# Optimization experiments

Measured on AMD Instinct MI355X. Metric: run time of the kernel, lower is better.

The kernel has to match this reference:

```python
import jax, jax.numpy as jnp
import numpy as np

T, B, DIM, N = 2048, 16, 1024, 64


def setup_inputs() -> dict:
    key = jax.random.key(0)
    ks = jax.random.split(key, 6)
    # xavier-uniform-ish scale for [N, DIM] linear weights
    lim = float(np.sqrt(6.0 / (DIM + N)))
    mk = lambda k: jax.random.uniform(k, (N, DIM), jnp.float32, -lim, lim)
    return {
        "x": jax.random.normal(ks[0], (T, B, DIM), jnp.float32),
        "S": jnp.zeros((B, N, N), jnp.float32),
        "W_k": mk(ks[1]),
        "W_v": mk(ks[2]),
        "W_q": mk(ks[3]),
        "W_alpha": mk(ks[4]),
        "d_alpha": jnp.full((N,), 0.1, jnp.float32),
        "b_alpha": jnp.full((N,), 2.0, jnp.float32),
    }


def reference(x, S, W_k, W_v, W_q, W_alpha, d_alpha, b_alpha):
    # Projections for the whole sequence at once: [T, B, N]
    k_all = jnp.einsum('tbd,nd->tbn', x, W_k)
    v_all = jnp.einsum('tbd,nd->tbn', x, W_v)
    q_all = jnp.einsum('tbd,nd->tbn', x, W_q)
    a_all = jnp.einsum('tbd,nd->tbn', x, W_alpha)

    def step(S, inp):
        k, v, q, ax = inp  # each [B, N]
        retrieved = jnp.einsum('bij,bj->bi', S, k)                 # [B, N]
        alpha = jax.nn.sigmoid(ax + d_alpha * retrieved + b_alpha)  # [B, N]
        outer_vk = v[:, :, None] * k[:, None, :]                    # [B, N, N]
        S = alpha[:, :, None] * S + (1.0 - alpha[:, :, None]) * outer_vk
        out = jnp.einsum('bij,bj->bi', S, q)                        # [B, N]
        out = out * jax.nn.silu(out)
        return S, out

    S_final, output = jax.lax.scan(step, S, (k_all, v_all, q_all, a_all))
    return output, S_final
```

## Files before the change

kernel.cpp:

```cpp
#include <hip/hip_runtime.h>
#include <hip/hip_bf16.h>

#define T_STEPS 2048
#define BATCH 16
#define DIM 1024
#define NDIM 64
#define M_TOTAL (T_STEPS * BATCH)
#define STRIDE (BATCH * NDIM)
#define CH 32

typedef __attribute__((ext_vector_type(8))) short bf16x8;
typedef __attribute__((ext_vector_type(4))) float f32x4;
typedef __attribute__((ext_vector_type(2))) float f32x2;

#define NEG_LOG2E -1.44269504088896f

__device__ inline unsigned pk_bf(float lo, float hi) {
    __hip_bfloat162 h = __float22bfloat162_rn(float2{lo, hi});
    return *(unsigned*)&h;
}

template <int CTRL>
__device__ inline float dpp_add(float x) {
    int v = __builtin_amdgcn_update_dpp(0, __float_as_int(x), CTRL, 0xF, 0xF, true);
    return x + __int_as_float(v);
}
__device__ inline float red16(float x) {
    x = dpp_add<0xB1>(x);
    x = dpp_add<0x4E>(x);
    x = dpp_add<0x141>(x);
    x = dpp_add<0x140>(x);
    return x;
}
__device__ inline void red16x2(float& a, float& b) {
    a = dpp_add<0xB1>(a);  b = dpp_add<0xB1>(b);
    a = dpp_add<0x4E>(a);  b = dpp_add<0x4E>(b);
    a = dpp_add<0x141>(a); b = dpp_add<0x141>(b);
    a = dpp_add<0x140>(a); b = dpp_add<0x140>(b);
}

#define AS1 __attribute__((address_space(1)))
#define AS3 __attribute__((address_space(3)))
__device__ inline void gl_lds16(const float* g, float* l) {
    __builtin_amdgcn_global_load_lds((const AS1 unsigned*)g, (AS3 unsigned*)l, 16, 0, 0);
}
__device__ inline void gl_lds16s(const unsigned short* g, unsigned short* l) {
    __builtin_amdgcn_global_load_lds((const AS1 unsigned*)g, (AS3 unsigned*)l, 16, 0, 0);
}
__device__ inline void gl_lds4(const float* g, float* l) {
    __builtin_amdgcn_global_load_lds((const AS1 unsigned*)g, (AS3 unsigned*)l, 4, 0, 0);
}
#define WAIT_VM0 do { __builtin_amdgcn_s_waitcnt(0x0F70); asm volatile("" ::: "memory"); } while (0)

__global__ __launch_bounds__(256) void pack_w(
    const float* __restrict__ Wk, const float* __restrict__ Wq,
    const float* __restrict__ Wv, const float* __restrict__ Wa,
    unsigned short* __restrict__ Wb) {
    int n = blockIdx.x;
    int sel = n >> 6;
    const float* W = (sel == 0) ? Wk : (sel == 1) ? Wq : (sel == 2) ? Wv : Wa;
    int k4 = threadIdx.x * 4;
    float4 f = *(const float4*)(W + (size_t)(n & 63) * DIM + k4);
    uint2 u;
    u.x = pk_bf(f.x, f.y);
    u.y = pk_bf(f.z, f.w);
    *(uint2*)(Wb + (size_t)n * DIM + k4) = u;
}

__global__ __launch_bounds__(256, 2) void proj_kernel(
    const float* __restrict__ x, const unsigned short* __restrict__ Wb,
    const float* __restrict__ ba, float* __restrict__ Kp, float* __restrict__ Qp,
    float* __restrict__ VAi) {
    __shared__ float sA[128 * 64];
    __shared__ unsigned short sB[128 * 64];

    const int m0 = blockIdx.x * 128;
    const int ntile = blockIdx.y;
    const int tid = threadIdx.x;
    const int wv = tid >> 6, lane = tid & 63, lrow = lane & 15, quad = lane >> 4;
    const int wm = wv & 1, wn = wv >> 1;

    f32x4 acc[4][4];
#pragma unroll
    for (int a = 0; a < 4; a++)
#pragma unroll
        for (int b = 0; b < 4; b++) acc[a][b] = (f32x4)(0.f);

    const float* xg = x + (size_t)(m0 + (tid >> 4)) * DIM + (tid & 15) * 4;
    const unsigned short* wg = Wb + (size_t)(ntile * 128 + (tid >> 3)) * DIM + (tid & 7) * 8;

    for (int it = 0; it < 16; ++it) {
        const int k0 = it * 64;
        __syncthreads();
#pragma unroll
        for (int j = 0; j < 8; ++j)
            gl_lds16(xg + (size_t)(16 * j) * DIM + k0, &sA[(tid + 256 * j) * 4]);
#pragma unroll
        for (int j = 0; j < 4; ++j)
            gl_lds16s(wg + (size_t)(32 * j) * DIM + k0, &sB[(tid + 256 * j) * 8]);
        WAIT_VM0;
        __syncthreads();

#pragma unroll
        for (int ks = 0; ks < 2; ++ks) {
            bf16x8 af[4];
#pragma unroll
            for (int mt = 0; mt < 4; ++mt) {
                const float* pa = &sA[(wm * 64 + mt * 16 + lrow) * 64 + ks * 32 + quad * 8];
                float4 lo = ((const float4*)pa)[0], hi = ((const float4*)pa)[1];
                unsigned pk[4] = {pk_bf(lo.x, lo.y), pk_bf(lo.z, lo.w),
                                  pk_bf(hi.x, hi.y), pk_bf(hi.z, hi.w)};
                af[mt] = *(bf16x8*)pk;
            }
#pragma unroll
            for (int nt = 0; nt < 4; ++nt) {
                bf16x8 bfr = *(const bf16x8*)&sB[(wn * 64 + nt * 16 + lrow) * 64 + ks * 32 + quad * 8];
#pragma unroll
                for (int mt = 0; mt < 4; ++mt)
                    acc[mt][nt] = __builtin_amdgcn_mfma_f32_16x16x32_bf16(af[mt], bfr, acc[mt][nt], 0, 0, 0);
            }
        }
    }

    const int g2 = ntile * 2 + wn;
    float bav[4];
    if (g2 == 3) {
#pragma unroll
        for (int nt = 0; nt < 4; ++nt) bav[nt] = ba[nt * 16 + lrow];
    }
#pragma unroll
    for (int mt = 0; mt < 4; ++mt)
#pragma unroll
        for (int nt = 0; nt < 4; ++nt) {
            int col = nt * 16 + lrow;
#pragma unroll
            for (int reg = 0; reg < 4; ++reg) {
                int m = m0 + wm * 64 + mt * 16 + quad * 4 + reg;
                float vvv = acc[mt][nt][reg];
                if (g2 == 0) Kp[(size_t)m * 64 + col] = vvv;
                else if (g2 == 1) Qp[(size_t)m * 64 + col] = vvv;
                else if (g2 == 2) VAi[(size_t)m * 128 + col * 2] = vvv;
                else VAi[(size_t)m * 128 + col * 2 + 1] = NEG_LOG2E * (vvv + bav[nt]);
            }
        }
}

__global__ __launch_bounds__(256) void kq_kernel(
    const float* __restrict__ Kp, const float* __restrict__ Qp, float* __restrict__ kq) {
    int m = blockIdx.x * 16 + (threadIdx.x >> 4);
    int c = threadIdx.x & 15;
    float4 k = *(const float4*)(Kp + (size_t)m * 64 + c * 4);
    float4 q = *(const float4*)(Qp + (size_t)m * 64 + c * 4);
    float p = k.x * q.x + k.y * q.y + k.z * q.z + k.w * q.w;
    p = red16(p);
    if (c == 0) kq[m] = p;
}

__global__ __launch_bounds__(256) void silu_kernel(float* __restrict__ out) {
    size_t idx = ((size_t)blockIdx.x * 256 + threadIdx.x) * 4;
    f32x4 o = *(const f32x4*)(out + idx);
    f32x4 rr;
#pragma unroll
    for (int j = 0; j < 4; ++j) {
        float e = __builtin_amdgcn_exp2f(o[j] * NEG_LOG2E);
        rr[j] = o[j] * o[j] * __builtin_amdgcn_rcpf(1.f + e);
    }
    *(f32x4*)(out + idx) = rr;
}

__global__ __launch_bounds__(64, 1) void recur_kernel(
    const float* __restrict__ Kp, const float* __restrict__ Qp,
    const float* __restrict__ VAi, const float* __restrict__ KQp,
    const float* __restrict__ S0, const float* __restrict__ d_alpha,
    float* __restrict__ out, float* __restrict__ Sout) {
    __shared__ float Kl[2][CH][64];
    __shared__ float Ql[2][CH][64];
    __shared__ float VAl[2][CH][8];
    __shared__ float KQl[2][64];
    __shared__ float Ol[CH][4];

    int b = blockIdx.y, g = blockIdx.x, lane = threadIdx.x;
    int r = lane >> 4, c = lane & 15, i = g * 4 + r, c4 = c * 4;

    float4 sv = *(const float4*)(S0 + ((size_t)b * NDIM + i) * NDIM + c4);
    f32x2 s01 = {sv.x, sv.y}, s23 = {sv.z, sv.w};
    float da2 = d_alpha[i] * NEG_LOG2E;

    const float* Kbase = Kp + (size_t)b * NDIM + (size_t)(lane >> 4) * STRIDE + (lane & 15) * 4;
    const float* Qbase = Qp + (size_t)b * NDIM + (size_t)(lane >> 4) * STRIDE + (lane & 15) * 4;
    const float* VAbase = VAi + (size_t)b * 128 + g * 8 + (lane & 1) * 4 + (size_t)(lane >> 1) * 2048;
    const float* KQbase = KQp + b + (size_t)(lane & 31) * BATCH;

    auto load_chunk = [&](int t0, int buf) {
#pragma unroll
        for (int j = 0; j < 8; ++j) {
            gl_lds16(Kbase + (size_t)(t0 + j * 4) * STRIDE, &Kl[buf][j * 4][0]);
            gl_lds16(Qbase + (size_t)(t0 + j * 4) * STRIDE, &Ql[buf][j * 4][0]);
        }
        gl_lds16(VAbase + (size_t)t0 * 2048, &VAl[buf][0][0]);
        gl_lds4(KQbase + (size_t)t0 * BATCH, &KQl[buf][0]);
    };

    load_chunk(0, 0);
    WAIT_VM0;

    f32x2 k01[2], k23[2], q01[2], q23[2], va[2];
    float kqv[2];
    {
        const float* Kb0 = &Kl[0][0][0] + c4;
        const float* Qb0 = &Ql[0][0][0] + c4;
#pragma unroll
        for (int u = 0; u < 2; ++u) {
            f32x4 kk_ = *(const f32x4*)(Kb0 + u * 64);
            f32x4 qq_ = *(const f32x4*)(Qb0 + u * 64);
            k01[u] = kk_.lo; k23[u] = kk_.hi;
            q01[u] = qq_.lo; q23[u] = qq_.hi;
            va[u] = *(const f32x2*)&VAl[0][u][r * 2];
            kqv[u] = KQl[0][u];
        }
    }

#define STEP(u, sl) do {                                                        \
    f32x2 k0v = k01[sl], k1v = k23[sl], q0v = q01[sl], q1v = q23[sl];           \
    f32x2 vva = va[sl];                                                         \
    float kqs = kqv[sl];                                                        \
    f32x4 kk_ = *(const f32x4*)(Kt + (u + 2) * 64);                             \
    f32x4 qq_ = *(const f32x4*)(Qt + (u + 2) * 64);                             \
    k01[sl] = kk_.lo; k23[sl] = kk_.hi;                                         \
    q01[sl] = qq_.lo; q23[sl] = qq_.hi;                                         \
    va[sl] = *(const f32x2*)(Vt + (u + 2) * 8);                                 \
    kqv[sl] = Qk[t4 + u + 2];                                                   \
    f32x2 pk_ = k0v * s01; pk_ = k1v * s23 + pk_;                               \
    f32x2 pq_ = q0v * s01; pq_ = q1v * s23 + pq_;                               \
    float rk_ = pk_.x + pk_.y, rq_ = pq_.x + pq_.y;                             \
    red16x2(rk_, rq_);                                                          \
    float v_ = vva.x;                                                           \
    f32x2 w01 = v_ * k0v, w23 = v_ * k1v;                                       \
    f32x2 d01 = s01 - w01, d23 = s23 - w23;                                     \
    float alpha_ = __builtin_amdgcn_rcpf(                                       \
        1.f + __builtin_amdgcn_exp2f(fmaf(da2, rk_, vva.y)));                   \
    f32x2 a2 = {alpha_, alpha_};                                                \
    s01 = w01 + a2 * d01;                                                       \
    s23 = w23 + a2 * d23;                                                       \
    float vkq_ = v_ * kqs;                                                      \
    float o_ = fmaf(alpha_, rq_ - vkq_, vkq_);                     \
    if (c == 0) Ol[t4 + u][r] = o_;                                             \
} while (0)

#pragma unroll 1
    for (int j = 0; j < T_STEPS / CH; ++j) {
        const int cb = j & 1, nb = cb ^ 1;
        if (j + 1 < T_STEPS / CH) load_chunk((j + 1) * CH, nb);

        const float* Kb = &Kl[cb][0][0] + c4;
        const float* Qb = &Ql[cb][0][0] + c4;
        const float* Vb = &VAl[cb][0][0] + r * 2;
        const float* Qk = &KQl[cb][0];

#pragma unroll 1
        for (int t4 = 0; t4 < CH; t4 += 4) {
            const float* Kt = Kb + t4 * 64;
            const float* Qt = Qb + t4 * 64;
            const float* Vt = Vb + t4 * 8;
            STEP(0, 0);
            STEP(1, 1);
            STEP(2, 0);
            STEP(3, 1);
        }
        WAIT_VM0;

        if (lane < 32) {
            float4 t4o = *(const float4*)&Ol[lane][0];
            *(float4*)(out + ((size_t)(j * CH + lane) * BATCH + b) * NDIM + g * 4) = t4o;
        }

        if (j + 1 < T_STEPS / CH) {
            const float* Kn = &Kl[nb][0][0] + c4;
            const float* Qn = &Ql[nb][0][0] + c4;
#pragma unroll
            for (int u = 0; u < 2; ++u) {
                f32x4 kk_ = *(const f32x4*)(Kn + u * 64);
                f32x4 qq_ = *(const f32x4*)(Qn + u * 64);
                k01[u] = kk_.lo; k23[u] = kk_.hi;
                q01[u] = qq_.lo; q23[u] = qq_.hi;
                va[u] = *(const f32x2*)&VAl[nb][u][r * 2];
                kqv[u] = KQl[nb][u];
            }
        }
    }
#undef STEP

    float* so_ = Sout + ((size_t)b * NDIM + i) * NDIM + c4;
    *(float4*)so_ = float4{s01.x, s01.y, s23.x, s23.y};
}

extern "C" void kernel_launch(void* const* d_in, const int* in_sizes, int n_in,
                              void* d_out, int out_size, void* d_ws, size_t ws_size,
                              hipStream_t stream) {
    const float* x  = (const float*)d_in[0];
    const float* S0 = (const float*)d_in[1];
    const float* Wk = (const float*)d_in[2];
    const float* Wv = (const float*)d_in[3];
    const float* Wq = (const float*)d_in[4];
    const float* Wa = (const float*)d_in[5];
    const float* da = (const float*)d_in[6];
    const float* ba = (const float*)d_in[7];

    float* out = (float*)d_out;
    float* Sout = out + (size_t)T_STEPS * BATCH * NDIM;

    const size_t per = (size_t)M_TOTAL * NDIM;
    float* Kp  = (float*)d_ws;
    float* Qp  = Kp + per;
    float* VAi = Qp + per;
    float* kq  = VAi + 2 * per;
    unsigned short* Wb = (unsigned short*)(kq + M_TOTAL);

    pack_w<<<dim3(256), dim3(256), 0, stream>>>(Wk, Wq, Wv, Wa, Wb);
    proj_kernel<<<dim3(M_TOTAL / 128, 2), dim3(256), 0, stream>>>(x, Wb, ba, Kp, Qp, VAi);
    kq_kernel<<<dim3(M_TOTAL / 16), dim3(256), 0, stream>>>(Kp, Qp, kq);
    recur_kernel<<<dim3(16, BATCH), dim3(64), 0, stream>>>(Kp, Qp, VAi, kq, S0, da, out, Sout);
    silu_kernel<<<dim3((T_STEPS * BATCH * NDIM) / (256 * 4)), dim3(256), 0, stream>>>(out);
}
```

Baseline: 507.5 us.

## Process two row groups per recurrence wavefront to increase ILP and halve blocks

Each recurrence wavefront now handles two 4-row groups of the state matrix (gA and gB = gA+8) instead of one, and the grid shrinks from 16×16 to 8×16 blocks. The K/Q chunks staged in LDS are shared by both groups, so their global loads are issued half as often. The two independent dependency chains interleave their DPP reductions and exp/rcp work, which can hide latency in the serial time loop. The cost is more registers and VALU work per step on a single wave, plus fewer waves in flight across the GPU.

```diff
diff --git a/kernel.cpp b/kernel.cpp
--- a/kernel.cpp
+++ b/kernel.cpp
@@ -32,11 +32,11 @@
     x = dpp_add<0x140>(x);
     return x;
 }
-__device__ inline void red16x2(float& a, float& b) {
-    a = dpp_add<0xB1>(a);  b = dpp_add<0xB1>(b);
-    a = dpp_add<0x4E>(a);  b = dpp_add<0x4E>(b);
-    a = dpp_add<0x141>(a); b = dpp_add<0x141>(b);
-    a = dpp_add<0x140>(a); b = dpp_add<0x140>(b);
+__device__ inline void red16x4(float& a, float& b, float& cc, float& d) {
+    a = dpp_add<0xB1>(a);  b = dpp_add<0xB1>(b);  cc = dpp_add<0xB1>(cc);  d = dpp_add<0xB1>(d);
+    a = dpp_add<0x4E>(a);  b = dpp_add<0x4E>(b);  cc = dpp_add<0x4E>(cc);  d = dpp_add<0x4E>(d);
+    a = dpp_add<0x141>(a); b = dpp_add<0x141>(b); cc = dpp_add<0x141>(cc); d = dpp_add<0x141>(d);
+    a = dpp_add<0x140>(a); b = dpp_add<0x140>(b); cc = dpp_add<0x140>(cc); d = dpp_add<0x140>(d);
 }
 
 #define AS1 __attribute__((address_space(1)))
@@ -175,20 +175,26 @@
     float* __restrict__ out, float* __restrict__ Sout) {
     __shared__ float Kl[2][CH][64];
     __shared__ float Ql[2][CH][64];
-    __shared__ float VAl[2][CH][8];
+    __shared__ float VAlA[2][CH][8];
+    __shared__ float VAlB[2][CH][8];
     __shared__ float KQl[2][64];
-    __shared__ float Ol[CH][4];
-
-    int b = blockIdx.y, g = blockIdx.x, lane = threadIdx.x;
-    int r = lane >> 4, c = lane & 15, i = g * 4 + r, c4 = c * 4;
-
-    float4 sv = *(const float4*)(S0 + ((size_t)b * NDIM + i) * NDIM + c4);
-    f32x2 s01 = {sv.x, sv.y}, s23 = {sv.z, sv.w};
-    float da2 = d_alpha[i] * NEG_LOG2E;
+    __shared__ float OlA[CH][4];
+    __shared__ float OlB[CH][4];
+
+    int b = blockIdx.y, gA = blockIdx.x, gB = gA + 8, lane = threadIdx.x;
+    int r = lane >> 4, c = lane & 15, c4 = c * 4;
+    int iA = gA * 4 + r, iB = gB * 4 + r;
+
+    f32x4 sA = *(const f32x4*)(S0 + ((size_t)b * NDIM + iA) * NDIM + c4);
+    f32x4 sB_ = *(const f32x4*)(S0 + ((size_t)b * NDIM + iB) * NDIM + c4);
+    f32x2 sA01 = sA.lo, sA23 = sA.hi, sB01 = sB_.lo, sB23 = sB_.hi;
+    float daA2 = d_alpha[iA] * NEG_LOG2E;
+    float daB2 = d_alpha[iB] * NEG_LOG2E;
 
     const float* Kbase = Kp + (size_t)b * NDIM + (size_t)(lane >> 4) * STRIDE + (lane & 15) * 4;
     const float* Qbase = Qp + (size_t)b * NDIM + (size_t)(lane >> 4) * STRIDE + (lane & 15) * 4;
-    const float* VAbase = VAi + (size_t)b * 128 + g * 8 + (lane & 1) * 4 + (size_t)(lane >> 1) * 2048;
+    const float* VAbaseA = VAi + (size_t)b * 128 + gA * 8 + (lane & 1) * 4 + (size_t)(lane >> 1) * 2048;
+    const float* VAbaseB = VAi + (size_t)b * 128 + gB * 8 + (lane & 1) * 4 + (size_t)(lane >> 1) * 2048;
     const float* KQbase = KQp + b + (size_t)(lane & 31) * BATCH;
 
     auto load_chunk = [&](int t0, int buf) {
@@ -197,14 +203,15 @@
             gl_lds16(Kbase + (size_t)(t0 + j * 4) * STRIDE, &Kl[buf][j * 4][0]);
             gl_lds16(Qbase + (size_t)(t0 + j * 4) * STRIDE, &Ql[buf][j * 4][0]);
         }
-        gl_lds16(VAbase + (size_t)t0 * 2048, &VAl[buf][0][0]);
+        gl_lds16(VAbaseA + (size_t)t0 * 2048, &VAlA[buf][0][0]);
+        gl_lds16(VAbaseB + (size_t)t0 * 2048, &VAlB[buf][0][0]);
         gl_lds4(KQbase + (size_t)t0 * BATCH, &KQl[buf][0]);
     };
 
     load_chunk(0, 0);
     WAIT_VM0;
 
-    f32x2 k01[2], k23[2], q01[2], q23[2], va[2];
+    f32x2 k01[2], k23[2], q01[2], q23[2], vaA[2], vaB[2];
     float kqv[2];
     {
         const float* Kb0 = &Kl[0][0][0] + c4;
@@ -215,36 +222,48 @@
             f32x4 qq_ = *(const f32x4*)(Qb0 + u * 64);
             k01[u] = kk_.lo; k23[u] = kk_.hi;
             q01[u] = qq_.lo; q23[u] = qq_.hi;
-            va[u] = *(const f32x2*)&VAl[0][u][r * 2];
+            vaA[u] = *(const f32x2*)&VAlA[0][u][r * 2];
+            vaB[u] = *(const f32x2*)&VAlB[0][u][r * 2];
             kqv[u] = KQl[0][u];
         }
     }
 
 #define STEP(u, sl) do {                                                        \
     f32x2 k0v = k01[sl], k1v = k23[sl], q0v = q01[sl], q1v = q23[sl];           \
-    f32x2 vva = va[sl];                                                         \
+    f32x2 vvaA = vaA[sl], vvaB = vaB[sl];                                       \
     float kqs = kqv[sl];                                                        \
     f32x4 kk_ = *(const f32x4*)(Kt + (u + 2) * 64);                             \
     f32x4 qq_ = *(const f32x4*)(Qt + (u + 2) * 64);                             \
     k01[sl] = kk_.lo; k23[sl] = kk_.hi;                                         \
     q01[sl] = qq_.lo; q23[sl] = qq_.hi;                                         \
-    va[sl] = *(const f32x2*)(Vt + (u + 2) * 8);                                 \
+    vaA[sl] = *(const f32x2*)(VtA + (u + 2) * 8);                               \
+    vaB[sl] = *(const f32x2*)(VtB + (u + 2) * 8);                               \
     kqv[sl] = Qk[t4 + u + 2];                                                   \
-    f32x2 pk_ = k0v * s01; pk_ = k1v * s23 + pk_;                               \
-    f32x2 pq_ = q0v * s01; pq_ = q1v * s23 + pq_;                               \
-    float rk_ = pk_.x + pk_.y, rq_ = pq_.x + pq_.y;                             \
-    red16x2(rk_, rq_);                                                          \
-    float v_ = vva.x;                                                           \
-    f32x2 w01 = v_ * k0v, w23 = v_ * k1v;                                       \
-    f32x2 d01 = s01 - w01, d23 = s23 - w23;                                     \
-    float alpha_ = __builtin_amdgcn_rcpf(                                       \
-        1.f + __builtin_amdgcn_exp2f(fmaf(da2, rk_, vva.y)));                   \
-    f32x2 a2 = {alpha_, alpha_};                                                \
-    s01 = w01 + a2 * d01;                                                       \
-    s23 = w23 + a2 * d23;                                                       \
-    float vkq_ = v_ * kqs;                                                      \
-    float o_ = fmaf(alpha_, rq_ - vkq_, vkq_);                     \
-    if (c == 0) Ol[t4 + u][r] = o_;                                             \
+    f32x2 pkA = k0v * sA01; pkA = k1v * sA23 + pkA;                             \
+    f32x2 pqA = q0v * sA01; pqA = q1v * sA23 + pqA;                             \
+    f32x2 pkB = k0v * sB01; pkB = k1v * sB23 + pkB;                             \
+    f32x2 pqB = q0v * sB01; pqB = q1v * sB23 + pqB;                             \
+    float rkA = pkA.x + pkA.y, rqA = pqA.x + pqA.y;                             \
+    float rkB = pkB.x + pkB.y, rqB = pqB.x + pqB.y;                             \
+    red16x4(rkA, rqA, rkB, rqB);                                                \
+    float vA_ = vvaA.x, vB_ = vvaB.x;                                           \
+    f32x2 wA01 = vA_ * k0v, wA23 = vA_ * k1v;                                   \
+    f32x2 wB01 = vB_ * k0v, wB23 = vB_ * k1v;                                   \
+    f32x2 dA01 = sA01 - wA01, dA23 = sA23 - wA23;                               \
+    f32x2 dB01 = sB01 - wB01, dB23 = sB23 - wB23;                               \
+    float alA = __builtin_amdgcn_rcpf(                                          \
+        1.f + __builtin_amdgcn_exp2f(fmaf(daA2, rkA, vvaA.y)));                 \
+    float alB = __builtin_amdgcn_rcpf(                                          \
+        1.f + __builtin_amdgcn_exp2f(fmaf(daB2, rkB, vvaB.y)));                 \
+    f32x2 aA = {alA, alA}, aB = {alB, alB};                                     \
+    sA01 = wA01 + aA * dA01;                                                    \
+    sA23 = wA23 + aA * dA23;                                                    \
+    sB01 = wB01 + aB * dB01;                                                    \
+    sB23 = wB23 + aB * dB23;                                                    \
+    float vkqA = vA_ * kqs, vkqB = vB_ * kqs;                                   \
+    float oA = fmaf(alA, rqA - vkqA, vkqA);                        \
+    float oB = fmaf(alB, rqB - vkqB, vkqB);                                     \
+    if (c == 0) { OlA[t4 + u][r] = oA; OlB[t4 + u][r] = oB; }                   \
 } while (0)
 
 #pragma unroll 1
@@ -254,14 +273,16 @@
 
         const float* Kb = &Kl[cb][0][0] + c4;
         const float* Qb = &Ql[cb][0][0] + c4;
-        const float* Vb = &VAl[cb][0][0] + r * 2;
+        const float* VbA = &VAlA[cb][0][0] + r * 2;
+        const float* VbB = &VAlB[cb][0][0] + r * 2;
         const float* Qk = &KQl[cb][0];
 
 #pragma unroll 1
         for (int t4 = 0; t4 < CH; t4 += 4) {
             const float* Kt = Kb + t4 * 64;
             const float* Qt = Qb + t4 * 64;
-            const float* Vt = Vb + t4 * 8;
+            const float* VtA = VbA + t4 * 8;
+            const float* VtB = VbB + t4 * 8;
             STEP(0, 0);
             STEP(1, 1);
             STEP(2, 0);
@@ -270,8 +291,11 @@
         WAIT_VM0;
 
         if (lane < 32) {
-            float4 t4o = *(const float4*)&Ol[lane][0];
-            *(float4*)(out + ((size_t)(j * CH + lane) * BATCH + b) * NDIM + g * 4) = t4o;
+            float4 tA = *(const float4*)&OlA[lane][0];
+            float4 tB = *(const float4*)&OlB[lane][0];
+            float* ob = out + ((size_t)(j * CH + lane) * BATCH + b) * NDIM;
+            *(float4*)(ob + gA * 4) = tA;
+            *(float4*)(ob + gB * 4) = tB;
         }
 
         if (j + 1 < T_STEPS / CH) {
@@ -283,15 +307,18 @@
                 f32x4 qq_ = *(const f32x4*)(Qn + u * 64);
                 k01[u] = kk_.lo; k23[u] = kk_.hi;
                 q01[u] = qq_.lo; q23[u] = qq_.hi;
-                va[u] = *(const f32x2*)&VAl[nb][u][r * 2];
+                vaA[u] = *(const f32x2*)&VAlA[nb][u][r * 2];
+                vaB[u] = *(const f32x2*)&VAlB[nb][u][r * 2];
                 kqv[u] = KQl[nb][u];
             }
         }
     }
 #undef STEP
 
-    float* so_ = Sout + ((size_t)b * NDIM + i) * NDIM + c4;
-    *(float4*)so_ = float4{s01.x, s01.y, s23.x, s23.y};
+    *(float4*)(Sout + ((size_t)b * NDIM + iA) * NDIM + c4) =
+        float4{sA01.x, sA01.y, sA23.x, sA23.y};
+    *(float4*)(Sout + ((size_t)b * NDIM + iB) * NDIM + c4) =
+        float4{sB01.x, sB01.y, sB23.x, sB23.y};
 }
 
 extern "C" void kernel_launch(void* const* d_in, const int* in_sizes, int n_in,
@@ -319,6 +346,6 @@
     pack_w<<<dim3(256), dim3(256), 0, stream>>>(Wk, Wq, Wv, Wa, Wb);
     proj_kernel<<<dim3(M_TOTAL / 128, 2), dim3(256), 0, stream>>>(x, Wb, ba, Kp, Qp, VAi);
     kq_kernel<<<dim3(M_TOTAL / 16), dim3(256), 0, stream>>>(Kp, Qp, kq);
-    recur_kernel<<<dim3(16, BATCH), dim3(64), 0, stream>>>(Kp, Qp, VAi, kq, S0, da, out, Sout);
+    recur_kernel<<<dim3(8, BATCH), dim3(64), 0, stream>>>(Kp, Qp, VAi, kq, S0, da, out, Sout);
     silu_kernel<<<dim3((T_STEPS * BATCH * NDIM) / (256 * 4)), dim3(256), 0, stream>>>(out);
 }
```

Result: slower. 580.5 us (+14.4%).

## Fuse weight packing, kq dot and SiLU into projection and recurrence kernels

Applied to the files above, without the earlier changes.

Drops the separate pack_w, kq_kernel and silu_kernel launches. The projection kernel now reads fp32 weights directly and converts them to bf16 from LDS, then computes the k·q dot product in its epilogue. SiLU is applied when the recurrence kernel writes its output. The recurrence inner loop is also restructured to double-buffer register groups of four timesteps instead of a rolling two-slot prefetch, and it writes the output transposed in LDS. The aim is to remove three launches and their extra global passes over Kp/Qp/out. The cost is doubled weight LDS/load traffic and extra conversion work in the projection, plus more register pressure in the recurrence.

```diff
diff --git a/kernel.cpp b/kernel.cpp
--- a/kernel.cpp
+++ b/kernel.cpp
@@ -38,41 +38,34 @@
     a = dpp_add<0x141>(a); b = dpp_add<0x141>(b);
     a = dpp_add<0x140>(a); b = dpp_add<0x140>(b);
 }
+__device__ inline float dot4(f32x4 a, f32x4 b) {
+    f32x2 t = a.lo * b.lo;
+    t = a.hi * b.hi + t;
+    return t.x + t.y;
+}
+__device__ inline float silu_o(float o) {
+    float e = __builtin_amdgcn_exp2f(o * NEG_LOG2E);
+    return o * o * __builtin_amdgcn_rcpf(1.f + e);
+}
 
 #define AS1 __attribute__((address_space(1)))
 #define AS3 __attribute__((address_space(3)))
 __device__ inline void gl_lds16(const float* g, float* l) {
     __builtin_amdgcn_global_load_lds((const AS1 unsigned*)g, (AS3 unsigned*)l, 16, 0, 0);
 }
-__device__ inline void gl_lds16s(const unsigned short* g, unsigned short* l) {
-    __builtin_amdgcn_global_load_lds((const AS1 unsigned*)g, (AS3 unsigned*)l, 16, 0, 0);
-}
 __device__ inline void gl_lds4(const float* g, float* l) {
     __builtin_amdgcn_global_load_lds((const AS1 unsigned*)g, (AS3 unsigned*)l, 4, 0, 0);
 }
 #define WAIT_VM0 do { __builtin_amdgcn_s_waitcnt(0x0F70); asm volatile("" ::: "memory"); } while (0)
 
-__global__ __launch_bounds__(256) void pack_w(
+__global__ __launch_bounds__(256, 2) void proj_kernel(
+    const float* __restrict__ x,
     const float* __restrict__ Wk, const float* __restrict__ Wq,
     const float* __restrict__ Wv, const float* __restrict__ Wa,
-    unsigned short* __restrict__ Wb) {
-    int n = blockIdx.x;
-    int sel = n >> 6;
-    const float* W = (sel == 0) ? Wk : (sel == 1) ? Wq : (sel == 2) ? Wv : Wa;
-    int k4 = threadIdx.x * 4;
-    float4 f = *(const float4*)(W + (size_t)(n & 63) * DIM + k4);
-    uint2 u;
-    u.x = pk_bf(f.x, f.y);
-    u.y = pk_bf(f.z, f.w);
-    *(uint2*)(Wb + (size_t)n * DIM + k4) = u;
-}
-
-__global__ __launch_bounds__(256, 2) void proj_kernel(
-    const float* __restrict__ x, const unsigned short* __restrict__ Wb,
     const float* __restrict__ ba, float* __restrict__ Kp, float* __restrict__ Qp,
-    float* __restrict__ VAi) {
+    float* __restrict__ VAi, float* __restrict__ kq) {
     __shared__ float sA[128 * 64];
-    __shared__ unsigned short sB[128 * 64];
+    __shared__ float sB[128 * 64];
 
     const int m0 = blockIdx.x * 128;
     const int ntile = blockIdx.y;
@@ -80,6 +73,9 @@
     const int wv = tid >> 6, lane = tid & 63, lrow = lane & 15, quad = lane >> 4;
     const int wm = wv & 1, wn = wv >> 1;
 
+    const float* w0 = (ntile == 0) ? Wk : Wv;
+    const float* w1 = (ntile == 0) ? Wq : Wa;
+
     f32x4 acc[4][4];
 #pragma unroll
     for (int a = 0; a < 4; a++)
@@ -87,7 +83,7 @@
         for (int b = 0; b < 4; b++) acc[a][b] = (f32x4)(0.f);
 
     const float* xg = x + (size_t)(m0 + (tid >> 4)) * DIM + (tid & 15) * 4;
-    const unsigned short* wg = Wb + (size_t)(ntile * 128 + (tid >> 3)) * DIM + (tid & 7) * 8;
+    const int wrow = tid >> 4, wcol = (tid & 15) * 4;
 
     for (int it = 0; it < 16; ++it) {
         const int k0 = it * 64;
@@ -97,7 +93,10 @@
             gl_lds16(xg + (size_t)(16 * j) * DIM + k0, &sA[(tid + 256 * j) * 4]);
 #pragma unroll
         for (int j = 0; j < 4; ++j)
-            gl_lds16s(wg + (size_t)(32 * j) * DIM + k0, &sB[(tid + 256 * j) * 8]);
+            gl_lds16(w0 + (size_t)(16 * j + wrow) * DIM + k0 + wcol, &sB[(tid + 256 * j) * 4]);
+#pragma unroll
+        for (int j = 0; j < 4; ++j)
+            gl_lds16(w1 + (size_t)(16 * j + wrow) * DIM + k0 + wcol, &sB[(tid + 256 * (j + 4)) * 4]);
         WAIT_VM0;
         __syncthreads();
 
@@ -114,7 +113,11 @@
             }
 #pragma unroll
             for (int nt = 0; nt < 4; ++nt) {
-                bf16x8 bfr = *(const bf16x8*)&sB[(wn * 64 + nt * 16 + lrow) * 64 + ks * 32 + quad * 8];
+                const float* pb = &sB[(wn * 64 + nt * 16 + lrow) * 64 + ks * 32 + quad * 8];
+                float4 lo = ((const float4*)pb)[0], hi = ((const float4*)pb)[1];
+                unsigned pk[4] = {pk_bf(lo.x, lo.y), pk_bf(lo.z, lo.w),
+                                  pk_bf(hi.x, hi.y), pk_bf(hi.z, hi.w)};
+                bf16x8 bfr = *(bf16x8*)pk;
 #pragma unroll
                 for (int mt = 0; mt < 4; ++mt)
                     acc[mt][nt] = __builtin_amdgcn_mfma_f32_16x16x32_bf16(af[mt], bfr, acc[mt][nt], 0, 0, 0);
@@ -143,29 +146,28 @@
                 else VAi[(size_t)m * 128 + col * 2 + 1] = NEG_LOG2E * (vvv + bav[nt]);
             }
         }
-}
-
-__global__ __launch_bounds__(256) void kq_kernel(
-    const float* __restrict__ Kp, const float* __restrict__ Qp, float* __restrict__ kq) {
-    int m = blockIdx.x * 16 + (threadIdx.x >> 4);
-    int c = threadIdx.x & 15;
-    float4 k = *(const float4*)(Kp + (size_t)m * 64 + c * 4);
-    float4 q = *(const float4*)(Qp + (size_t)m * 64 + c * 4);
-    float p = k.x * q.x + k.y * q.y + k.z * q.z + k.w * q.w;
-    p = red16(p);
-    if (c == 0) kq[m] = p;
-}
-
-__global__ __launch_bounds__(256) void silu_kernel(float* __restrict__ out) {
-    size_t idx = ((size_t)blockIdx.x * 256 + threadIdx.x) * 4;
-    f32x4 o = *(const f32x4*)(out + idx);
-    f32x4 rr;
-#pragma unroll
-    for (int j = 0; j < 4; ++j) {
-        float e = __builtin_amdgcn_exp2f(o[j] * NEG_LOG2E);
-        rr[j] = o[j] * o[j] * __builtin_amdgcn_rcpf(1.f + e);
+
+    if (ntile == 0) {
+        __syncthreads();
+        float* dst = (wn == 0) ? sA : sB;
+#pragma unroll
+        for (int mt = 0; mt < 4; ++mt)
+#pragma unroll
+            for (int nt = 0; nt < 4; ++nt)
+#pragma unroll
+                for (int reg = 0; reg < 4; ++reg)
+                    dst[(wm * 64 + mt * 16 + quad * 4 + reg) * 64 + nt * 16 + lrow] =
+                        acc[mt][nt][reg];
+        __syncthreads();
+        if (tid < 128) {
+            float s = 0.f;
+#pragma unroll
+            for (int k4 = 0; k4 < 16; ++k4)
+                s += dot4(*(const f32x4*)&sA[tid * 64 + k4 * 4],
+                          *(const f32x4*)&sB[tid * 64 + k4 * 4]);
+            kq[m0 + tid] = s;
+        }
     }
-    *(f32x4*)(out + idx) = rr;
 }
 
 __global__ __launch_bounds__(64, 1) void recur_kernel(
@@ -177,13 +179,12 @@
     __shared__ float Ql[2][CH][64];
     __shared__ float VAl[2][CH][8];
     __shared__ float KQl[2][64];
-    __shared__ float Ol[CH][4];
+    __shared__ float OlT[4][CH];
 
     int b = blockIdx.y, g = blockIdx.x, lane = threadIdx.x;
     int r = lane >> 4, c = lane & 15, i = g * 4 + r, c4 = c * 4;
 
-    float4 sv = *(const float4*)(S0 + ((size_t)b * NDIM + i) * NDIM + c4);
-    f32x2 s01 = {sv.x, sv.y}, s23 = {sv.z, sv.w};
+    f32x4 sv = *(const f32x4*)(S0 + ((size_t)b * NDIM + i) * NDIM + c4);
     float da2 = d_alpha[i] * NEG_LOG2E;
 
     const float* Kbase = Kp + (size_t)b * NDIM + (size_t)(lane >> 4) * STRIDE + (lane & 15) * 4;
@@ -201,97 +202,75 @@
         gl_lds4(KQbase + (size_t)t0 * BATCH, &KQl[buf][0]);
     };
 
+    f32x4 kg[2][4], qg[2][4], kqg[2];
+    f32x2 vg[2][4];
+    f32x4 og;
+
+#define LOADG(gi, buf, t4_) do {                                         \
+    const float* Kb_ = &Kl[buf][0][0] + (t4_) * 64 + c4;                 \
+    const float* Qb_ = &Ql[buf][0][0] + (t4_) * 64 + c4;                 \
+    _Pragma("unroll")                                                    \
+    for (int u_ = 0; u_ < 4; ++u_) {                                     \
+        kg[gi][u_] = *(const f32x4*)(Kb_ + u_ * 64);                     \
+        qg[gi][u_] = *(const f32x4*)(Qb_ + u_ * 64);                     \
+        vg[gi][u_] = *(const f32x2*)(&VAl[buf][0][0] + ((t4_) + u_) * 8 + r * 2); \
+    }                                                                    \
+    kqg[gi] = *(const f32x4*)(&KQl[buf][0] + (t4_));                     \
+} while (0)
+
+#define STEP(gi, u) do {                                                 \
+    f32x4 kv_ = kg[gi][u], qv_ = qg[gi][u];                              \
+    f32x2 vva_ = vg[gi][u];                                              \
+    float kqs_ = kqg[gi][u];                                             \
+    f32x2 pk_ = kv_.lo * sv.lo; pk_ = kv_.hi * sv.hi + pk_;              \
+    f32x2 pq_ = qv_.lo * sv.lo; pq_ = qv_.hi * sv.hi + pq_;              \
+    float rk_ = pk_.x + pk_.y, rq_ = pq_.x + pq_.y;                      \
+    red16x2(rk_, rq_);                                                   \
+    float v_ = vva_.x;                                                   \
+    f32x4 w_ = v_ * kv_;                                                 \
+    f32x4 d_ = sv - w_;                                                  \
+    float alpha_ = __builtin_amdgcn_rcpf(                                \
+        1.f + __builtin_amdgcn_exp2f(fmaf(da2, rk_, vva_.y)));           \
+    sv = w_ + alpha_ * d_;                                               \
+    float vkq_ = v_ * kqs_;                                              \
+    og[u] = fmaf(alpha_, rq_ - vkq_, vkq_);                 \
+} while (0)
+
     load_chunk(0, 0);
     WAIT_VM0;
-
-    f32x2 k01[2], k23[2], q01[2], q23[2], va[2];
-    float kqv[2];
-    {
-        const float* Kb0 = &Kl[0][0][0] + c4;
-        const float* Qb0 = &Ql[0][0][0] + c4;
-#pragma unroll
-        for (int u = 0; u < 2; ++u) {
-            f32x4 kk_ = *(const f32x4*)(Kb0 + u * 64);
-            f32x4 qq_ = *(const f32x4*)(Qb0 + u * 64);
-            k01[u] = kk_.lo; k23[u] = kk_.hi;
-            q01[u] = qq_.lo; q23[u] = qq_.hi;
-            va[u] = *(const f32x2*)&VAl[0][u][r * 2];
-            kqv[u] = KQl[0][u];
-        }
-    }
-
-#define STEP(u, sl) do {                                                        \
-    f32x2 k0v = k01[sl], k1v = k23[sl], q0v = q01[sl], q1v = q23[sl];           \
-    f32x2 vva = va[sl];                                                         \
-    float kqs = kqv[sl];                                                        \
-    f32x4 kk_ = *(const f32x4*)(Kt + (u + 2) * 64);                             \
-    f32x4 qq_ = *(const f32x4*)(Qt + (u + 2) * 64);                             \
-    k01[sl] = kk_.lo; k23[sl] = kk_.hi;                                         \
-    q01[sl] = qq_.lo; q23[sl] = qq_.hi;                                         \
-    va[sl] = *(const f32x2*)(Vt + (u + 2) * 8);                                 \
-    kqv[sl] = Qk[t4 + u + 2];                                                   \
-    f32x2 pk_ = k0v * s01; pk_ = k1v * s23 + pk_;                               \
-    f32x2 pq_ = q0v * s01; pq_ = q1v * s23 + pq_;                               \
-    float rk_ = pk_.x + pk_.y, rq_ = pq_.x + pq_.y;                             \
-    red16x2(rk_, rq_);                                                          \
-    float v_ = vva.x;                                                           \
-    f32x2 w01 = v_ * k0v, w23 = v_ * k1v;                                       \
-    f32x2 d01 = s01 - w01, d23 = s23 - w23;                                     \
-    float alpha_ = __builtin_amdgcn_rcpf(                                       \
-        1.f + __builtin_amdgcn_exp2f(fmaf(da2, rk_, vva.y)));                   \
-    f32x2 a2 = {alpha_, alpha_};                                                \
-    s01 = w01 + a2 * d01;                                                       \
-    s23 = w23 + a2 * d23;                                                       \
-    float vkq_ = v_ * kqs;                                                      \
-    float o_ = fmaf(alpha_, rq_ - vkq_, vkq_);                     \
-    if (c == 0) Ol[t4 + u][r] = o_;                                             \
-} while (0)
+    LOADG(0, 0, 0);
 
 #pragma unroll 1
     for (int j = 0; j < T_STEPS / CH; ++j) {
         const int cb = j & 1, nb = cb ^ 1;
         if (j + 1 < T_STEPS / CH) load_chunk((j + 1) * CH, nb);
 
-        const float* Kb = &Kl[cb][0][0] + c4;
-        const float* Qb = &Ql[cb][0][0] + c4;
-        const float* Vb = &VAl[cb][0][0] + r * 2;
-        const float* Qk = &KQl[cb][0];
-
 #pragma unroll 1
-        for (int t4 = 0; t4 < CH; t4 += 4) {
-            const float* Kt = Kb + t4 * 64;
-            const float* Qt = Qb + t4 * 64;
-            const float* Vt = Vb + t4 * 8;
-            STEP(0, 0);
-            STEP(1, 1);
-            STEP(2, 0);
-            STEP(3, 1);
+        for (int t8 = 0; t8 < CH; t8 += 8) {
+            LOADG(1, cb, t8 + 4);
+            STEP(0, 0); STEP(0, 1); STEP(0, 2); STEP(0, 3);
+            if (c == 0) *(f32x4*)(&OlT[r][t8]) = og;
+            if (t8 + 8 < CH) LOADG(0, cb, t8 + 8);
+            STEP(1, 0); STEP(1, 1); STEP(1, 2); STEP(1, 3);
+            if (c == 0) *(f32x4*)(&OlT[r][t8 + 4]) = og;
         }
         WAIT_VM0;
 
         if (lane < 32) {
-            float4 t4o = *(const float4*)&Ol[lane][0];
+            float4 t4o;
+            t4o.x = silu_o(OlT[0][lane]);
+            t4o.y = silu_o(OlT[1][lane]);
+            t4o.z = silu_o(OlT[2][lane]);
+            t4o.w = silu_o(OlT[3][lane]);
             *(float4*)(out + ((size_t)(j * CH + lane) * BATCH + b) * NDIM + g * 4) = t4o;
         }
 
-        if (j + 1 < T_STEPS / CH) {
-            const float* Kn = &Kl[nb][0][0] + c4;
-            const float* Qn = &Ql[nb][0][0] + c4;
-#pragma unroll
-            for (int u = 0; u < 2; ++u) {
-                f32x4 kk_ = *(const f32x4*)(Kn + u * 64);
-                f32x4 qq_ = *(const f32x4*)(Qn + u * 64);
-                k01[u] = kk_.lo; k23[u] = kk_.hi;
-                q01[u] = qq_.lo; q23[u] = qq_.hi;
-                va[u] = *(const f32x2*)&VAl[nb][u][r * 2];
-                kqv[u] = KQl[nb][u];
-            }
-        }
+        if (j + 1 < T_STEPS / CH) LOADG(0, nb, 0);
     }
 #undef STEP
-
-    float* so_ = Sout + ((size_t)b * NDIM + i) * NDIM + c4;
-    *(float4*)so_ = float4{s01.x, s01.y, s23.x, s23.y};
+#undef LOADG
+
+    *(float4*)(Sout + ((size_t)b * NDIM + i) * NDIM + c4) = float4{sv.x, sv.y, sv.z, sv.w};
 }
 
 extern "C" void kernel_launch(void* const* d_in, const int* in_sizes, int n_in,
@@ -314,11 +293,8 @@
     float* Qp  = Kp + per;
     float* VAi = Qp + per;
     float* kq  = VAi + 2 * per;
-    unsigned short* Wb = (unsigned short*)(kq + M_TOTAL);
-
-    pack_w<<<dim3(256), dim3(256), 0, stream>>>(Wk, Wq, Wv, Wa, Wb);
-    proj_kernel<<<dim3(M_TOTAL / 128, 2), dim3(256), 0, stream>>>(x, Wb, ba, Kp, Qp, VAi);
-    kq_kernel<<<dim3(M_TOTAL / 16), dim3(256), 0, stream>>>(Kp, Qp, kq);
+
+    proj_kernel<<<dim3(M_TOTAL / 128, 2), dim3(256), 0, stream>>>(
+        x, Wk, Wq, Wv, Wa, ba, Kp, Qp, VAi, kq);
     recur_kernel<<<dim3(16, BATCH), dim3(64), 0, stream>>>(Kp, Qp, VAi, kq, S0, da, out, Sout);
-    silu_kernel<<<dim3((T_STEPS * BATCH * NDIM) / (256 * 4)), dim3(256), 0, stream>>>(out);
-}
+}
```

After: 451.2 us. -11.1%, faster.
